# Kernel tuning notes

Hardware: AMD Instinct MI355X
Metric: run time of the kernel (lower is better)

The kernel has to match this reference:

```python
import jax, jax.numpy as jnp
import numpy as np
import math

D = 1024            # model dim
H = 4               # gru heads
HD = D // H         # 256 head dim
DI = int(HD * 1.5)  # 384 minGRU inner dim (expansion_factor=1.5)
FF_INNER = int(D * 4 * 2 / 3)  # 2730 SwiGLU inner
K = 4               # causal depthwise conv kernel
RES_SCALE = 1.0     # 1/sqrt(num_layers=1)


def setup_inputs() -> dict:
    key = jax.random.key(0)
    ks = jax.random.split(key, 12)
    s = lambda k, shape, sc: jax.random.normal(k, shape, jnp.float32) * sc
    return {
        "x": s(ks[0], (4, 4096, D), 1.0),
        "dw_w": s(ks[1], (D, 1, K), 0.3),
        "dw_b": jnp.zeros((D,), jnp.float32),
        "pw_w": s(ks[2], (D, D), 1.0 / math.sqrt(D)),
        "pw_b": jnp.zeros((D,), jnp.float32),
        "conv_gamma": jnp.zeros((D,), jnp.float32),
        "gru_gamma": jnp.zeros((D,), jnp.float32),
        "ff_gamma": jnp.zeros((D,), jnp.float32),
        "w_hg": s(ks[3], (H, HD, 2 * DI), 1.0 / math.sqrt(HD)),
        "w_out": s(ks[4], (H, DI, HD), 1.0 / math.sqrt(DI)),
        "w_gate": s(ks[5], (D, FF_INNER), 1.0 / math.sqrt(D)),
        "w_value": s(ks[6], (D, FF_INNER), 1.0 / math.sqrt(D)),
        "w_ff_out": s(ks[7], (FF_INNER, D), 1.0 / math.sqrt(FF_INNER)),
    }


def _rmsnorm(x, gamma):
    # F.normalize(x, dim=-1) * sqrt(dim) * (gamma + 1)
    n = jnp.sqrt(jnp.sum(x * x, axis=-1, keepdims=True))
    return x / jnp.maximum(n, 1e-12) * math.sqrt(x.shape[-1]) * (gamma + 1.0)


def _log_g(x):
    return jnp.where(x >= 0, jnp.log(jax.nn.relu(x) + 0.5), -jax.nn.softplus(-x))


def _causal_conv(x, dw_w, dw_b, pw_w, pw_b):
    # x: [B,L,D] -> causal depthwise conv (k=K) -> pointwise 1x1
    xt = jnp.transpose(x, (0, 2, 1))  # [B,D,L]
    xt = jnp.pad(xt, ((0, 0), (0, 0), (K - 1, 0)))
    y = jax.lax.conv_general_dilated(
        xt, dw_w, (1,), "VALID",
        dimension_numbers=("NCH", "OIH", "NCH"),
        feature_group_count=D) + dw_b[None, :, None]
    y = jnp.einsum("bdl,ed->bel", y, pw_w) + pw_b[None, :, None]
    return jnp.transpose(y, (0, 2, 1))


def reference(x, dw_w, dw_b, pw_w, pw_b, conv_gamma, gru_gamma, ff_gamma,
              w_hg, w_out, w_gate, w_value, w_ff_out):
    B, L, _ = x.shape
    # conv residual branch
    x = _causal_conv(_rmsnorm(x, conv_gamma), dw_w, dw_b, pw_w, pw_b) * RES_SCALE + x
    # multi-head minGRU (all heads vectorized; prev_hidden=None)
    normed = _rmsnorm(x, gru_gamma).reshape(B, L, H, HD)
    hg = jnp.einsum("blhd,hde->blhe", normed, w_hg)  # [B,L,H,2*DI]
    hidden, gate = hg[..., :DI], hg[..., DI:]
    log_coeffs = -jax.nn.softplus(gate)
    log_values = -jax.nn.softplus(-gate) + _log_g(hidden)
    # heinsen associative scan in log space along L
    a_star = jnp.cumsum(log_coeffs, axis=1)
    log_h = a_star + jax.lax.cumlogsumexp(log_values - a_star, axis=1)
    h = jnp.exp(log_h)  # [B,L,H,DI]
    next_hidden = h[:, -1:].reshape(B, 1, H * DI)
    gru_out = jnp.einsum("blhe,heo->blho", h, w_out).reshape(B, L, D)
    x = gru_out * RES_SCALE + x
    # SwiGLU FFN residual branch
    n = _rmsnorm(x, ff_gamma)
    ff = (jax.nn.silu(n @ w_gate) * (n @ w_value)) @ w_ff_out
    x = ff * RES_SCALE + x
    return x, next_hidden
```

## Files before the change

### kernel.cpp

```cpp
#include <hip/hip_runtime.h>
#include <stdint.h>


#define DM     1024
#define SEQL   4096
#define FFN    2730
#define FFP    2816
#define NH_OFF 16777216L
#define CHLEN  128

using bf16x8 = __attribute__((ext_vector_type(8))) short;
using f32x4  = __attribute__((ext_vector_type(4))) float;

__device__ __forceinline__ float bf2f(unsigned short h) {
  union { unsigned int u; float f; } v; v.u = ((unsigned int)h) << 16; return v.f;
}
__device__ __forceinline__ unsigned short f2bf(float f) {
  union { float f; unsigned int u; } v; v.f = f;
  unsigned int u = v.u;
  return (unsigned short)((u + 0x7fffu + ((u >> 16) & 1u)) >> 16);
}
__device__ __forceinline__ float ldin(const void* p, long i, int f32mode) {
  return f32mode ? ((const float*)p)[i] : bf2f(((const unsigned short*)p)[i]);
}
__device__ __forceinline__ void stout(void* p, long i, int f32mode, float v) {
  if (f32mode) ((float*)p)[i] = v; else ((unsigned short*)p)[i] = f2bf(v);
}
__device__ __forceinline__ void gload_lds16(const unsigned short* g, unsigned short* lds) {
  __builtin_amdgcn_global_load_lds(
      (const __attribute__((address_space(1))) unsigned int*)g,
      (__attribute__((address_space(3))) unsigned int*)lds,
      16, 0, 0);
}

__global__ void detect_k(const unsigned short* __restrict__ x, int* __restrict__ flag) {
  __shared__ int cnt;
  if (threadIdx.x == 0) cnt = 0;
  __syncthreads();
  int c = 0;
  for (int j = 0; j < 4; j++) {
    unsigned short v = x[2 * (threadIdx.x * 4 + j)];
    int ex = (v >> 7) & 0xFF;
    if (ex >= 0x84) c++;
  }
  atomicAdd(&cnt, c);
  __syncthreads();
  if (threadIdx.x == 0) *flag = (cnt >= 32) ? 1 : 0;
}

template <int EPI>
__launch_bounds__(256)
__global__ void gemm_bf16(const unsigned short* __restrict__ A, int lda, int aOffZ,
                          const unsigned short* __restrict__ Bm, int bOffZ, int K,
                          void* __restrict__ Cout, int ldc, int cOffZ, long outOff,
                          const unsigned short* __restrict__ bias,
                          const void* __restrict__ res, int ldres, long resOff,
                          const int* __restrict__ flagp) {
  __shared__ __align__(16) unsigned short As[128][64];
  __shared__ __align__(16) unsigned short Bs[128][64];

  const int tid  = threadIdx.x;
  const int w    = tid >> 6;
  const int lane = tid & 63;
  const int z    = blockIdx.z;
  const long tm  = (long)blockIdx.y * 128;
  const long tn  = (long)blockIdx.x * 128;

  const unsigned short* Ag = A + (long)z * aOffZ;
  const unsigned short* Bg = Bm + (long)z * bOffZ;

  f32x4 acc[4][4];
#pragma unroll
  for (int i = 0; i < 4; i++)
#pragma unroll
    for (int j = 0; j < 4; j++) acc[i][j] = (f32x4){0.f, 0.f, 0.f, 0.f};

  const int wrow = w * 32;
  const int srow = lane >> 3;
  const int scol = (((lane & 7) ^ srow) * 8);
  const int wm   = (w >> 1) * 64;
  const int wn   = (w & 1) * 64;
  const int quad = lane >> 4;
  const int lo   = lane & 15;
  const int sw   = lo & 7;

  for (int k0 = 0; k0 < K; k0 += 64) {
    __syncthreads();
#pragma unroll
    for (int i = 0; i < 4; i++) {
      const int r = wrow + i * 8;
      gload_lds16(Ag + (tm + r + srow) * (long)lda + k0 + scol, &As[r][0]);
      gload_lds16(Bg + (tn + r + srow) * (long)K + k0 + scol, &Bs[r][0]);
    }
    __syncthreads();
#pragma unroll
    for (int kk = 0; kk < 64; kk += 32) {
      const int kc = kk >> 3;
      bf16x8 af[4], bfr[4];
#pragma unroll
      for (int mt = 0; mt < 4; mt++)
        af[mt] = *(const bf16x8*)&As[wm + mt * 16 + lo][((quad + kc) ^ sw) * 8];
#pragma unroll
      for (int nt = 0; nt < 4; nt++)
        bfr[nt] = *(const bf16x8*)&Bs[wn + nt * 16 + lo][((quad + kc) ^ sw) * 8];
#pragma unroll
      for (int mt = 0; mt < 4; mt++)
#pragma unroll
        for (int nt = 0; nt < 4; nt++)
          acc[mt][nt] = __builtin_amdgcn_mfma_f32_16x16x32_bf16(af[mt], bfr[nt], acc[mt][nt], 0, 0, 0);
    }
  }

  const int f32m = (EPI == 1 || EPI == 3) ? *flagp : 0;
#pragma unroll
  for (int mt = 0; mt < 4; mt++) {
#pragma unroll
    for (int nt = 0; nt < 4; nt++) {
#pragma unroll
      for (int r = 0; r < 4; r++) {
        const long grow = tm + wm + mt * 16 + quad * 4 + r;
        const long gcol = tn + wn + nt * 16 + lo;
        float v         = acc[mt][nt][r];
        if (EPI == 0) {
          ((unsigned short*)Cout + (long)z * cOffZ)[grow * (long)ldc + gcol] = f2bf(v);
        } else if (EPI == 1) {
          v += bf2f(bias[gcol]) + ldin(res, resOff + grow * (long)ldres + gcol, f32m);
          ((unsigned short*)Cout)[grow * (long)ldc + gcol] = f2bf(v);
        } else if (EPI == 2) {
          v += bf2f(((const unsigned short*)res + (long)z * cOffZ)[grow * (long)ldres + gcol]);
          ((unsigned short*)Cout + (long)z * cOffZ)[grow * (long)ldc + gcol] = f2bf(v);
        } else {
          v += bf2f(((const unsigned short*)res)[grow * (long)ldres + gcol]);
          stout(Cout, outOff + grow * (long)ldc + gcol, f32m, v);
        }
      }
    }
  }
}

__launch_bounds__(256)
__global__ void gemm_ff(const unsigned short* __restrict__ A,
                        const unsigned short* __restrict__ Bgm,
                        const unsigned short* __restrict__ Bvm,
                        unsigned short* __restrict__ Cout) {
  __shared__ __align__(16) unsigned short As[128][64];
  __shared__ __align__(16) unsigned short Bgs[128][64];
  __shared__ __align__(16) unsigned short Bvs[128][64];

  const int tid  = threadIdx.x;
  const int w    = tid >> 6;
  const int lane = tid & 63;
  const long tm  = (long)blockIdx.y * 128;
  const long tn  = (long)blockIdx.x * 128;

  f32x4 accG[4][4], accV[4][4];
#pragma unroll
  for (int i = 0; i < 4; i++)
#pragma unroll
    for (int j = 0; j < 4; j++) {
      accG[i][j] = (f32x4){0.f, 0.f, 0.f, 0.f};
      accV[i][j] = (f32x4){0.f, 0.f, 0.f, 0.f};
    }

  const int wrow = w * 32;
  const int srow = lane >> 3;
  const int scol = (((lane & 7) ^ srow) * 8);
  const int wm   = (w >> 1) * 64;
  const int wn   = (w & 1) * 64;
  const int quad = lane >> 4;
  const int lo   = lane & 15;
  const int sw   = lo & 7;

  for (int k0 = 0; k0 < DM; k0 += 64) {
    __syncthreads();
#pragma unroll
    for (int i = 0; i < 4; i++) {
      const int r = wrow + i * 8;
      gload_lds16(A + (tm + r + srow) * (long)DM + k0 + scol, &As[r][0]);
      gload_lds16(Bgm + (tn + r + srow) * (long)DM + k0 + scol, &Bgs[r][0]);
      gload_lds16(Bvm + (tn + r + srow) * (long)DM + k0 + scol, &Bvs[r][0]);
    }
    __syncthreads();
#pragma unroll
    for (int kk = 0; kk < 64; kk += 32) {
      const int kc = kk >> 3;
      bf16x8 af[4], bfr[4];
#pragma unroll
      for (int mt = 0; mt < 4; mt++)
        af[mt] = *(const bf16x8*)&As[wm + mt * 16 + lo][((quad + kc) ^ sw) * 8];
#pragma unroll
      for (int nt = 0; nt < 4; nt++)
        bfr[nt] = *(const bf16x8*)&Bgs[wn + nt * 16 + lo][((quad + kc) ^ sw) * 8];
#pragma unroll
      for (int mt = 0; mt < 4; mt++)
#pragma unroll
        for (int nt = 0; nt < 4; nt++)
          accG[mt][nt] = __builtin_amdgcn_mfma_f32_16x16x32_bf16(af[mt], bfr[nt], accG[mt][nt], 0, 0, 0);
#pragma unroll
      for (int nt = 0; nt < 4; nt++)
        bfr[nt] = *(const bf16x8*)&Bvs[wn + nt * 16 + lo][((quad + kc) ^ sw) * 8];
#pragma unroll
      for (int mt = 0; mt < 4; mt++)
#pragma unroll
        for (int nt = 0; nt < 4; nt++)
          accV[mt][nt] = __builtin_amdgcn_mfma_f32_16x16x32_bf16(af[mt], bfr[nt], accV[mt][nt], 0, 0, 0);
    }
  }

#pragma unroll
  for (int mt = 0; mt < 4; mt++) {
#pragma unroll
    for (int nt = 0; nt < 4; nt++) {
#pragma unroll
      for (int r = 0; r < 4; r++) {
        const long grow = tm + wm + mt * 16 + quad * 4 + r;
        const long gcol = tn + wn + nt * 16 + lo;
        const float g   = accG[mt][nt][r];
        const float s   = g / (1.f + __expf(-g));
        Cout[grow * (long)FFP + gcol] = f2bf(s * accV[mt][nt][r]);
      }
    }
  }
}

template <int EPI>
__launch_bounds__(512, 2)
__global__ void gemm256(const unsigned short* __restrict__ A,
                        const unsigned short* __restrict__ Bm,
                        int K,
                        void* __restrict__ Cout,
                        const unsigned short* __restrict__ res,
                        long outOff,
                        const int* __restrict__ flagp) {
  __shared__ __align__(16) unsigned short As[2][256][64];
  __shared__ __align__(16) unsigned short Bs[2][256][64];

  const int tid  = threadIdx.x;
  const int w    = tid >> 6;
  const int lane = tid & 63;
  const int wr   = w >> 2;
  const int wc   = w & 3;
  const int quad = lane >> 4;
  const int lo   = lane & 15;
  const int sw   = lo & 7;

  const int gx  = gridDim.x;
  int bid       = blockIdx.y * gx + blockIdx.x;
  const int nwg = gx * gridDim.y;
  {
    const int q = nwg >> 3, r8 = nwg & 7;
    const int xc8 = bid & 7, j = bid >> 3;
    bid = (xc8 < r8 ? xc8 * (q + 1) : r8 * (q + 1) + (xc8 - r8) * q) + j;
  }
  const long tn = (long)(bid % gx) * 256;
  const long tm = (long)(bid / gx) * 256;

  const int NT = K >> 6;

  const int srow = lane >> 3;
  const int sch  = (lane & 7) ^ srow;
  const unsigned short* Ab = A + (tm + (long)w * 8 + srow) * (long)K + sch * 8;
  const unsigned short* Bb = Bm + (tn + (long)w * 8 + srow) * (long)K + sch * 8;

#define STAGE_A(BUF, TT, G) \
  gload_lds16(Ab + (long)((G) * 64) * K + (long)(TT) * 64, &As[BUF][(G) * 64 + w * 8][0])
#define STAGE_B(BUF, TT, G) \
  gload_lds16(Bb + (long)((G) * 64) * K + (long)(TT) * 64, &Bs[BUF][(G) * 64 + w * 8][0])

  STAGE_A(0, 0, 0); STAGE_A(0, 0, 2);
  STAGE_B(0, 0, 0); STAGE_B(0, 0, 1);
  STAGE_A(0, 0, 1); STAGE_A(0, 0, 3);
  STAGE_B(0, 0, 2); STAGE_B(0, 0, 3);
  STAGE_A(1, 1, 0); STAGE_A(1, 1, 2);
  STAGE_B(1, 1, 0); STAGE_B(1, 1, 1);
  STAGE_A(1, 1, 1); STAGE_A(1, 1, 3);

  f32x4 acc[8][4];
#pragma unroll
  for (int i = 0; i < 8; i++)
#pragma unroll
    for (int j = 0; j < 4; j++) acc[i][j] = (f32x4){0.f, 0.f, 0.f, 0.f};

  asm volatile("s_waitcnt vmcnt(6)" ::: "memory");
  __builtin_amdgcn_s_barrier();

  bf16x8 a[4][2], b[4][2];

#define LDA256(CBUF, base_row)                                                    \
  _Pragma("unroll") for (int m = 0; m < 4; m++) {                                 \
    _Pragma("unroll") for (int c = 0; c < 2; c++) {                               \
      a[m][c] = *(const bf16x8*)&As[CBUF][(base_row) + m * 16 + lo]               \
                                       [((quad + 4 * c) ^ sw) * 8];               \
    }                                                                             \
  }
#define LDB256(CBUF, nb)                                                          \
  _Pragma("unroll") for (int n = 0; n < 2; n++) {                                 \
    _Pragma("unroll") for (int c = 0; c < 2; c++) {                               \
      b[(nb) + n][c] = *(const bf16x8*)&Bs[CBUF][wc * 64 + ((nb) + n) * 16 + lo]  \
                                              [((quad + 4 * c) ^ sw) * 8];        \
    }                                                                             \
  }
#define MFMA16(MB, NB)                                                            \
  __builtin_amdgcn_s_setprio(1);                                                  \
  _Pragma("unroll") for (int m = 0; m < 4; m++) {                                 \
    _Pragma("unroll") for (int n = 0; n < 2; n++) {                               \
      _Pragma("unroll") for (int c = 0; c < 2; c++) {                             \
        acc[(MB) + m][(NB) + n] = __builtin_amdgcn_mfma_f32_16x16x32_bf16(        \
            a[m][c], b[(NB) + n][c], acc[(MB) + m][(NB) + n], 0, 0, 0);           \
      }                                                                           \
    }                                                                             \
  }                                                                               \
  __builtin_amdgcn_s_setprio(0);

#define SUBTILE(CBUF, TT, ST1, ST2, LAST)                                         \
  {                                                                               \
                                                                         \
    LDA256(CBUF, wr * 128);                                                       \
    LDB256(CBUF, 0);                                                              \
    if (ST1) { STAGE_B(CBUF ^ 1, (TT) + 1, 2); STAGE_B(CBUF ^ 1, (TT) + 1, 3); }  \
    MFMA16(0, 0);                                                                 \
    __builtin_amdgcn_s_barrier();                                                 \
                                                                         \
    LDB256(CBUF, 2);                                                              \
    if (ST2) { STAGE_A(CBUF, (TT) + 2, 0); STAGE_A(CBUF, (TT) + 2, 2); }          \
    MFMA16(0, 2);                                                                 \
    __builtin_amdgcn_s_barrier();                                                 \
                                                                         \
    LDA256(CBUF, wr * 128 + 64);                                                  \
    if (ST2) { STAGE_B(CBUF, (TT) + 2, 0); STAGE_B(CBUF, (TT) + 2, 1); }          \
    MFMA16(4, 2);                                                                 \
    __builtin_amdgcn_s_barrier();                                                 \
                                                                         \
    if (ST2) { STAGE_A(CBUF, (TT) + 2, 1); STAGE_A(CBUF, (TT) + 2, 3); }          \
    MFMA16(4, 0);                                                                 \
    if (LAST) asm volatile("s_waitcnt vmcnt(0)" ::: "memory");                    \
    else      asm volatile("s_waitcnt vmcnt(6)" ::: "memory");                    \
    __builtin_amdgcn_s_barrier();                                                 \
  }

  for (int t = 0; t + 3 < NT; t += 2) {
    SUBTILE(0, t, 1, 1, 0)
    SUBTILE(1, t + 1, 1, 1, 0)
  }
  SUBTILE(0, NT - 2, 1, 0, 1)
  SUBTILE(1, NT - 1, 0, 0, 1)

  if (EPI == 0) {
    const long colb = (tn >> 1);
    const long rowb = tm + wr * 128;
#pragma unroll
    for (int m = 0; m < 8; m++) {
#pragma unroll
      for (int np = 0; np < 2; np++) {
        const long col = colb + (wc * 2 + np) * 16 + lo;
#pragma unroll
        for (int r = 0; r < 4; r++) {
          const long row = rowb + m * 16 + quad * 4 + r;
          const float g  = acc[m][2 * np][r];
          const float v  = acc[m][2 * np + 1][r];
          const float s  = g / (1.f + __expf(-g));
          ((unsigned short*)Cout)[row * (long)FFP + col] = f2bf(s * v);
        }
      }
    }
  } else {
    const int f32m = *flagp;
    const long rowb = tm + wr * 128;
    const long colb = tn + wc * 64;
#pragma unroll
    for (int m = 0; m < 8; m++) {
#pragma unroll
      for (int n = 0; n < 4; n++) {
#pragma unroll
        for (int r = 0; r < 4; r++) {
          const long row = rowb + m * 16 + quad * 4 + r;
          const long col = colb + n * 16 + lo;
          float v = acc[m][n][r] + bf2f(res[row * (long)DM + col]);
          stout(Cout, outOff + row * (long)DM + col, f32m, v);
        }
      }
    }
  }
#undef STAGE_A
#undef STAGE_B
#undef LDA256
#undef LDB256
#undef MFMA16
#undef SUBTILE
}

__global__ void rmsnorm_x(const void* __restrict__ in, long elemOff,
                          const unsigned short* __restrict__ gamma,
                          unsigned short* __restrict__ out,
                          const int* __restrict__ flagp) {
  const int t    = blockIdx.x;
  const int lane = threadIdx.x;
  const int f32m = *flagp;
  float v[16];
  const long base = elemOff + (long)t * DM;
  if (f32m) {
    const float4* rp = (const float4*)((const float*)in + base);
#pragma unroll
    for (int j = 0; j < 4; j++) {
      float4 u     = rp[j * 64 + lane];
      v[j * 4 + 0] = u.x; v[j * 4 + 1] = u.y; v[j * 4 + 2] = u.z; v[j * 4 + 3] = u.w;
    }
  } else {
    const ushort4* rp = (const ushort4*)((const unsigned short*)in + base);
#pragma unroll
    for (int j = 0; j < 4; j++) {
      ushort4 u    = rp[j * 64 + lane];
      v[j * 4 + 0] = bf2f(u.x); v[j * 4 + 1] = bf2f(u.y);
      v[j * 4 + 2] = bf2f(u.z); v[j * 4 + 3] = bf2f(u.w);
    }
  }
  float s = 0.f;
#pragma unroll
  for (int i = 0; i < 16; i++) s = fmaf(v[i], v[i], s);
#pragma unroll
  for (int off = 32; off > 0; off >>= 1) s += __shfl_xor(s, off, 64);
  const float scale = 32.f / fmaxf(sqrtf(s), 1e-12f);
  ushort4* op       = (ushort4*)(out + (long)t * DM);
  const ushort4* gp = (const ushort4*)gamma;
#pragma unroll
  for (int j = 0; j < 4; j++) {
    ushort4 g = gp[j * 64 + lane];
    ushort4 o;
    o.x = f2bf(v[j * 4 + 0] * scale * (bf2f(g.x) + 1.f));
    o.y = f2bf(v[j * 4 + 1] * scale * (bf2f(g.y) + 1.f));
    o.z = f2bf(v[j * 4 + 2] * scale * (bf2f(g.z) + 1.f));
    o.w = f2bf(v[j * 4 + 3] * scale * (bf2f(g.w) + 1.f));
    op[j * 64 + lane] = o;
  }
}

__global__ void rmsnorm_k(const unsigned short* __restrict__ in,
                          const unsigned short* __restrict__ gamma,
                          unsigned short* __restrict__ out) {
  const int t    = blockIdx.x;
  const int lane = threadIdx.x;
  float v[16];
  const ushort4* rp = (const ushort4*)(in + (long)t * DM);
#pragma unroll
  for (int j = 0; j < 4; j++) {
    ushort4 u    = rp[j * 64 + lane];
    v[j * 4 + 0] = bf2f(u.x); v[j * 4 + 1] = bf2f(u.y);
    v[j * 4 + 2] = bf2f(u.z); v[j * 4 + 3] = bf2f(u.w);
  }
  float s = 0.f;
#pragma unroll
  for (int i = 0; i < 16; i++) s = fmaf(v[i], v[i], s);
#pragma unroll
  for (int off = 32; off > 0; off >>= 1) s += __shfl_xor(s, off, 64);
  const float scale = 32.f / fmaxf(sqrtf(s), 1e-12f);
  ushort4* op       = (ushort4*)(out + (long)t * DM);
  const ushort4* gp = (const ushort4*)gamma;
#pragma unroll
  for (int j = 0; j < 4; j++) {
    ushort4 g = gp[j * 64 + lane];
    ushort4 o;
    o.x = f2bf(v[j * 4 + 0] * scale * (bf2f(g.x) + 1.f));
    o.y = f2bf(v[j * 4 + 1] * scale * (bf2f(g.y) + 1.f));
    o.z = f2bf(v[j * 4 + 2] * scale * (bf2f(g.z) + 1.f));
    o.w = f2bf(v[j * 4 + 3] * scale * (bf2f(g.w) + 1.f));
    op[j * 64 + lane] = o;
  }
}

__global__ void dwconv_k(const unsigned short* __restrict__ xn,
                         const unsigned short* __restrict__ dww,
                         const unsigned short* __restrict__ dwb,
                         unsigned short* __restrict__ y, int l0) {
  const int t = blockIdx.x;
  const int d = blockIdx.y * 256 + threadIdx.x;
  const int l = l0 + (t & (SEQL - 1));
  ushort4 w4  = ((const ushort4*)dww)[d];
  float wk[4] = {bf2f(w4.x), bf2f(w4.y), bf2f(w4.z), bf2f(w4.w)};
  float acc   = bf2f(dwb[d]);
#pragma unroll
  for (int k = 0; k < 4; k++) {
    const int ll = l + k - 3;
    if (ll >= 0) acc = fmaf(bf2f(xn[(long)(t + k - 3) * DM + d]), wk[k], acc);
  }
  y[(long)t * DM + d] = f2bf(acc);
}

__device__ __forceinline__ void cv_compute(float gt, float& c, float& sg) {
  gt = fminf(fmaxf(gt, -40.f), 40.f);
  const float e  = __expf(-fabsf(gt));
  const float r  = 1.f / (1.f + e);
  const float rs = e * r;
  c  = (gt >= 0.f) ? rs : r;
  sg = (gt >= 0.f) ? r : rs;
}
__device__ __forceinline__ float gfun(float hid) {
  hid = fminf(fmaxf(hid, -40.f), 40.f);
  if (hid >= 0.f) return hid + 0.5f;
  const float e = __expf(hid);
  return e / (1.f + e);
}

__global__ void scan_p1(const unsigned short* __restrict__ hg, float* __restrict__ cC,
                        float* __restrict__ cV, int chTot, int SL) {
  const int e = threadIdx.x, bh = blockIdx.y, cid = blockIdx.x;
  const int bL = bh >> 2, hh = bh & 3;
  long base = ((long)(bL * SL + cid * CHLEN)) * 3072 + hh * 768 + e;
  float C = 1.f, V = 0.f;
  for (int i = 0; i < CHLEN; i++) {
    const float hid = bf2f(hg[base]), gt = bf2f(hg[base + 384]);
    float c, sg; cv_compute(gt, c, sg);
    C *= c;
    V = fmaf(c, V, sg * gfun(hid));
    base += 3072;
  }
  const int idx = cid * chTot + bh * 384 + e;
  cC[idx] = C; cV[idx] = V;
}

__global__ void scan_p2(const float* __restrict__ cC, const float* __restrict__ cV,
                        float* __restrict__ hin, int chTot, int CHNp,
                        const float* __restrict__ hcarry, int useCarry) {
  const int ch = blockIdx.x * 384 + threadIdx.x;
  float h = useCarry ? hcarry[ch] : 0.f;
  for (int cid = 0; cid < CHNp; cid++) {
    const int idx = cid * chTot + ch;
    hin[idx] = h;
    h = fmaf(cC[idx], h, cV[idx]);
  }
}

__global__ void scan_p3(const unsigned short* __restrict__ hg, const float* __restrict__ hin,
                        unsigned short* __restrict__ hout, void* __restrict__ nh, long nhOff,
                        float* __restrict__ hcarry, int chTot, int SL, int CHNp,
                        int writeNh, const int* __restrict__ flagp) {
  const int e = threadIdx.x, bh = blockIdx.y, cid = blockIdx.x;
  const int bL = bh >> 2, hh = bh & 3;
  const long tok = (long)bL * SL + (long)cid * CHLEN;
  long base  = tok * 3072 + hh * 768 + e;
  long obase = tok * 1536 + hh * 384 + e;
  float h = hin[cid * chTot + bh * 384 + e];
  for (int i = 0; i < CHLEN; i++) {
    const float hid = bf2f(hg[base]), gt = bf2f(hg[base + 384]);
    float c, sg; cv_compute(gt, c, sg);
    h = fmaf(c, h, sg * gfun(hid));
    hout[obase] = f2bf(h);
    base += 3072; obase += 1536;
  }
  if (cid == CHNp - 1) {
    hcarry[bh * 384 + e] = h;
    if (writeNh) stout(nh, nhOff + bL * 1536 + hh * 384 + e, *flagp, h);
  }
}

__global__ void cvt_k(const void* __restrict__ in, unsigned short* __restrict__ out,
                      int n, const int* __restrict__ flagp) {
  const int i = blockIdx.x * 256 + threadIdx.x;
  if (i < n) out[i] = f2bf(ldin(in, i, *flagp));
}
__global__ void tr_whg(const void* __restrict__ in, unsigned short* __restrict__ out,
                       const int* __restrict__ flagp) {
  const int idx = blockIdx.x * 256 + threadIdx.x;
  const int k = idx & 255, n = (idx >> 8) % 768, h = idx / (768 * 256);
  out[idx] = f2bf(ldin(in, (long)(h * 256 + k) * 768 + n, *flagp));
}
__global__ void tr_wout(const void* __restrict__ in, unsigned short* __restrict__ out,
                        const int* __restrict__ flagp) {
  const int idx = blockIdx.x * 256 + threadIdx.x;
  const int k = idx % 384, n = (idx / 384) & 255, h = idx / (384 * 256);
  out[idx] = f2bf(ldin(in, (long)(h * 384 + k) * 256 + n, *flagp));
}
__global__ void tr_wg(const void* __restrict__ in, unsigned short* __restrict__ out,
                      const int* __restrict__ flagp) {
  const int idx = blockIdx.x * 256 + threadIdx.x;
  const int k = idx & 1023, n = idx >> 10;
  out[idx] = (n < FFN) ? f2bf(ldin(in, (long)k * FFN + n, *flagp)) : (unsigned short)0;
}
__global__ void tr_wgv(const void* __restrict__ wg, const void* __restrict__ wv,
                       unsigned short* __restrict__ out, const int* __restrict__ flagp) {
  const int idx = blockIdx.x * 256 + threadIdx.x;
  const int k = idx & 1023, R = idx >> 10;
  const int tile = R >> 8, rb = R & 255;
  const int pair = rb >> 5, sel = (rb >> 4) & 1, r16 = rb & 15;
  const int col  = tile * 128 + pair * 16 + r16;
  const void* src = sel ? wv : wg;
  out[idx] = (col < FFN) ? f2bf(ldin(src, (long)k * FFN + col, *flagp)) : (unsigned short)0;
}
__global__ void tr_wfo(const void* __restrict__ in, unsigned short* __restrict__ out,
                       const int* __restrict__ flagp) {
  const int idx = blockIdx.x * 256 + threadIdx.x;
  const int kk = idx % FFP, n = idx / FFP;
  out[idx] = (kk < FFN) ? f2bf(ldin(in, (long)kk * DM + n, *flagp)) : (unsigned short)0;
}

extern "C" void kernel_launch(void* const* d_in, const int* in_sizes, int n_in,
                              void* d_out, int out_size, void* d_ws, size_t ws_size,
                              hipStream_t stream) {
  const void* x      = d_in[0];
  const void* dw_w   = d_in[1];
  const void* dw_b   = d_in[2];
  const void* pw_w   = d_in[3];
  const void* pw_b   = d_in[4];
  const void* conv_g = d_in[5];
  const void* gru_g  = d_in[6];
  const void* ff_g   = d_in[7];
  const void* w_hg   = d_in[8];
  const void* w_out  = d_in[9];
  const void* w_gate = d_in[10];
  const void* w_val  = d_in[11];
  const void* w_ffo  = d_in[12];

  const long FIXED = 21795072L;
  int MT = 128;
  if      (ws_size >= (size_t)(FIXED + 16384L * 13888)) MT = 16384;
  else if (ws_size >= (size_t)(FIXED + 8192L * 13888))  MT = 8192;
  else if (ws_size >= (size_t)(FIXED + 4096L * 13888))  MT = 4096;
  else if (ws_size >= (size_t)(FIXED + 2048L * 13888))  MT = 2048;
  else if (ws_size >= (size_t)(FIXED + 1024L * 13888))  MT = 1024;
  else if (ws_size >= (size_t)(FIXED + 512L * 13888))   MT = 512;
  else if (ws_size >= (size_t)(FIXED + 256L * 13888))   MT = 256;

  const int SL    = (MT >= SEQL) ? SEQL : MT;
  const int nSeq  = MT / SL;
  const int CHNp  = SL / CHLEN;
  const int chTot = nSeq * 1536;
  const int big   = (MT >= 256);

  char* p = (char*)d_ws;
  unsigned short* whgT  = (unsigned short*)p; p += 1572864;
  unsigned short* woutT = (unsigned short*)p; p += 786432;
  unsigned short* wgT   = (unsigned short*)p; p += 5767168;
  unsigned short* wvT   = (unsigned short*)p; p += 5767168;
  unsigned short* wfoT  = (unsigned short*)p; p += 5767168;
  unsigned short* pwT   = (unsigned short*)p; p += 2097152;
  unsigned short* dwwB  = (unsigned short*)p; p += 8192;
  unsigned short* dwbB  = (unsigned short*)p; p += 2048;
  unsigned short* pwbB  = (unsigned short*)p; p += 2048;
  unsigned short* cgB   = (unsigned short*)p; p += 2048;
  unsigned short* ggB   = (unsigned short*)p; p += 2048;
  unsigned short* fgB   = (unsigned short*)p; p += 2048;
  int*            flag  = (int*)p;            p += 256;
  float*          hcarry= (float*)p;          p += 12288;
  float*          cC    = (float*)p;          p += (long)MT * 192;
  float*          cV    = (float*)p;          p += (long)MT * 192;
  float*          hin   = (float*)p;          p += (long)MT * 192;
  unsigned short* xnb   = (unsigned short*)p; p += 6144 + (long)MT * 2048;
  unsigned short* xc    = (unsigned short*)p; p += (long)MT * 2048;
  unsigned short* hbuf  = (unsigned short*)p; p += (long)MT * 3072;
  unsigned short* ybuf  = (unsigned short*)p;
  unsigned short* hg    = (unsigned short*)p;
  unsigned short* ffin  = (unsigned short*)p;
  unsigned short* xn    = xnb + 3 * DM;
  unsigned short* wgvT  = wgT;

  detect_k<<<1, 256, 0, stream>>>((const unsigned short*)x, flag);
  tr_whg<<<3072, 256, 0, stream>>>(w_hg, whgT, flag);
  tr_wout<<<1536, 256, 0, stream>>>(w_out, woutT, flag);
  if (big) {
    tr_wgv<<<22528, 256, 0, stream>>>(w_gate, w_val, wgvT, flag);
  } else {
    tr_wg<<<11264, 256, 0, stream>>>(w_gate, wgT, flag);
    tr_wg<<<11264, 256, 0, stream>>>(w_val, wvT, flag);
  }
  tr_wfo<<<11264, 256, 0, stream>>>(w_ffo, wfoT, flag);
  cvt_k<<<4096, 256, 0, stream>>>(pw_w, pwT, 1048576, flag);
  cvt_k<<<16, 256, 0, stream>>>(dw_w, dwwB, 4096, flag);
  cvt_k<<<4, 256, 0, stream>>>(dw_b, dwbB, 1024, flag);
  cvt_k<<<4, 256, 0, stream>>>(pw_b, pwbB, 1024, flag);
  cvt_k<<<4, 256, 0, stream>>>(conv_g, cgB, 1024, flag);
  cvt_k<<<4, 256, 0, stream>>>(gru_g, ggB, 1024, flag);
  cvt_k<<<4, 256, 0, stream>>>(ff_g, fgB, 1024, flag);

  for (long t0 = 0; t0 < 16384; t0 += MT) {
    const int l0     = (int)(t0 & (SEQL - 1));
    const int P      = (l0 > 0) ? 3 : 0;
    const int seqEnd = (l0 + SL == SEQL);
    const long nhOff = NH_OFF + (t0 / SEQL) * 1536;

    rmsnorm_x<<<MT + P, 64, 0, stream>>>(x, (t0 - P) * DM, cgB, xn - (long)P * DM, flag);
    dwconv_k<<<dim3(MT, 4), 256, 0, stream>>>(xn, dwwB, dwbB, ybuf, l0);
    gemm_bf16<1><<<dim3(8, MT / 128, 1), 256, 0, stream>>>(ybuf, DM, 0, pwT, 0, DM,
        xc, DM, 0, 0L, pwbB, x, DM, t0 * DM, flag);

    rmsnorm_k<<<MT, 64, 0, stream>>>(xc, ggB, xn);
    gemm_bf16<0><<<dim3(6, MT / 128, 4), 256, 0, stream>>>(xn, DM, 256, whgT, 196608, 256,
        hg, 3072, 768, 0L, nullptr, nullptr, 0, 0L, nullptr);
    scan_p1<<<dim3(CHNp, nSeq * 4), 384, 0, stream>>>(hg, cC, cV, chTot, SL);
    scan_p2<<<nSeq * 4, 384, 0, stream>>>(cC, cV, hin, chTot, CHNp, hcarry, l0 > 0);
    scan_p3<<<dim3(CHNp, nSeq * 4), 384, 0, stream>>>(hg, hin, hbuf, d_out, nhOff,
        hcarry, chTot, SL, CHNp, seqEnd, flag);
    gemm_bf16<2><<<dim3(2, MT / 128, 4), 256, 0, stream>>>(hbuf, 1536, 384, woutT, 98304, 384,
        xc, DM, 256, 0L, nullptr, xc, DM, 0L, nullptr);

    rmsnorm_k<<<MT, 64, 0, stream>>>(xc, fgB, xn);
    if (big) {
      gemm256<0><<<dim3(22, MT / 256), 512, 0, stream>>>(xn, wgvT, DM,
          ffin, nullptr, 0L, nullptr);
      gemm256<1><<<dim3(4, MT / 256), 512, 0, stream>>>(ffin, wfoT, FFP,
          d_out, xc, t0 * DM, flag);
    } else {
      gemm_ff<<<dim3(22, MT / 128), 256, 0, stream>>>(xn, wgT, wvT, ffin);
      gemm_bf16<3><<<dim3(8, MT / 128, 1), 256, 0, stream>>>(ffin, FFP, 0, wfoT, 0, FFP,
          d_out, DM, 0, t0 * DM, nullptr, xc, DM, 0L, flag);
    }
  }
}
```

Before: 975.2 us.

## Restructure GEMM main loop to prefetch LDS fragments across subtiles

Reworks the 256x256 GEMM inner loop to keep separate A-low, A-high and two B fragment register sets. Each quarter's LDS reads are issued while the previous quarter's MFMAs run, and the next buffer's first fragments are prefetched at the end of each subtile. Global-to-LDS staging is reordered so whole A then whole B tiles land per phase, with adjusted vmcnt waits. This aims to hide LDS read latency behind MFMA work, at the cost of more VGPRs and more delicate wait/barrier ordering.

```diff
diff --git a/kernel.cpp b/kernel.cpp
--- a/kernel.cpp
+++ b/kernel.cpp
@@ -268,12 +268,11 @@
   gload_lds16(Bb + (long)((G) * 64) * K + (long)(TT) * 64, &Bs[BUF][(G) * 64 + w * 8][0])
 
   STAGE_A(0, 0, 0); STAGE_A(0, 0, 2);
-  STAGE_B(0, 0, 0); STAGE_B(0, 0, 1);
   STAGE_A(0, 0, 1); STAGE_A(0, 0, 3);
-  STAGE_B(0, 0, 2); STAGE_B(0, 0, 3);
+  STAGE_B(0, 0, 0); STAGE_B(0, 0, 1); STAGE_B(0, 0, 2); STAGE_B(0, 0, 3);
   STAGE_A(1, 1, 0); STAGE_A(1, 1, 2);
-  STAGE_B(1, 1, 0); STAGE_B(1, 1, 1);
   STAGE_A(1, 1, 1); STAGE_A(1, 1, 3);
+  STAGE_B(1, 1, 0); STAGE_B(1, 1, 1); STAGE_B(1, 1, 2); STAGE_B(1, 1, 3);
 
   f32x4 acc[8][4];
 #pragma unroll
@@ -281,69 +280,91 @@
 #pragma unroll
     for (int j = 0; j < 4; j++) acc[i][j] = (f32x4){0.f, 0.f, 0.f, 0.f};
 
-  asm volatile("s_waitcnt vmcnt(6)" ::: "memory");
+  asm volatile("s_waitcnt vmcnt(8)" ::: "memory");
   __builtin_amdgcn_s_barrier();
 
-  bf16x8 a[4][2], b[4][2];
-
-#define LDA256(CBUF, base_row)                                                    \
+  bf16x8 aL[4][2], aH[4][2], b01[2][2], b23[2][2];
+
+#define LDAL(CBUF)                                                                \
   _Pragma("unroll") for (int m = 0; m < 4; m++) {                                 \
     _Pragma("unroll") for (int c = 0; c < 2; c++) {                               \
-      a[m][c] = *(const bf16x8*)&As[CBUF][(base_row) + m * 16 + lo]               \
-                                       [((quad + 4 * c) ^ sw) * 8];               \
+      aL[m][c] = *(const bf16x8*)&As[CBUF][wr * 128 + m * 16 + lo]                \
+                                        [((quad + 4 * c) ^ sw) * 8];              \
     }                                                                             \
   }
-#define LDB256(CBUF, nb)                                                          \
+#define LDAH(CBUF)                                                                \
+  _Pragma("unroll") for (int m = 0; m < 4; m++) {                                 \
+    _Pragma("unroll") for (int c = 0; c < 2; c++) {                               \
+      aH[m][c] = *(const bf16x8*)&As[CBUF][wr * 128 + 64 + m * 16 + lo]           \
+                                        [((quad + 4 * c) ^ sw) * 8];              \
+    }                                                                             \
+  }
+#define LDB01(CBUF)                                                               \
   _Pragma("unroll") for (int n = 0; n < 2; n++) {                                 \
     _Pragma("unroll") for (int c = 0; c < 2; c++) {                               \
-      b[(nb) + n][c] = *(const bf16x8*)&Bs[CBUF][wc * 64 + ((nb) + n) * 16 + lo]  \
-                                              [((quad + 4 * c) ^ sw) * 8];        \
+      b01[n][c] = *(const bf16x8*)&Bs[CBUF][wc * 64 + n * 16 + lo]                \
+                                         [((quad + 4 * c) ^ sw) * 8];             \
     }                                                                             \
   }
-#define MFMA16(MB, NB)                                                            \
+#define LDB23(CBUF)                                                               \
+  _Pragma("unroll") for (int n = 0; n < 2; n++) {                                 \
+    _Pragma("unroll") for (int c = 0; c < 2; c++) {                               \
+      b23[n][c] = *(const bf16x8*)&Bs[CBUF][wc * 64 + 32 + n * 16 + lo]           \
+                                         [((quad + 4 * c) ^ sw) * 8];             \
+    }                                                                             \
+  }
+#define MFMA_Q(MB, AF, NB, BF)                                                    \
   __builtin_amdgcn_s_setprio(1);                                                  \
   _Pragma("unroll") for (int m = 0; m < 4; m++) {                                 \
     _Pragma("unroll") for (int n = 0; n < 2; n++) {                               \
       _Pragma("unroll") for (int c = 0; c < 2; c++) {                             \
         acc[(MB) + m][(NB) + n] = __builtin_amdgcn_mfma_f32_16x16x32_bf16(        \
-            a[m][c], b[(NB) + n][c], acc[(MB) + m][(NB) + n], 0, 0, 0);           \
+            AF[m][c], BF[n][c], acc[(MB) + m][(NB) + n], 0, 0, 0);                \
       }                                                                           \
     }                                                                             \
   }                                                                               \
   __builtin_amdgcn_s_setprio(0);
 
-#define SUBTILE(CBUF, TT, ST1, ST2, LAST)                                         \
+#define LGKM0 asm volatile("s_waitcnt lgkmcnt(0)" ::: "memory")
+
+#define SUBTILE(CBUF, TT, STG, PRF, VM)                                           \
   {                                                                               \
-                                                                         \
-    LDA256(CBUF, wr * 128);                                                       \
-    LDB256(CBUF, 0);                                                              \
-    if (ST1) { STAGE_B(CBUF ^ 1, (TT) + 1, 2); STAGE_B(CBUF ^ 1, (TT) + 1, 3); }  \
-    MFMA16(0, 0);                                                                 \
+                                                            \
+    LGKM0;                                                                        \
+    if (STG) { STAGE_A(CBUF, (TT) + 2, 0); STAGE_A(CBUF, (TT) + 2, 2); }          \
+    MFMA_Q(0, aL, 0, b01);                                                        \
+    LDAH(CBUF);                                                                   \
     __builtin_amdgcn_s_barrier();                                                 \
-                                                                         \
-    LDB256(CBUF, 2);                                                              \
-    if (ST2) { STAGE_A(CBUF, (TT) + 2, 0); STAGE_A(CBUF, (TT) + 2, 2); }          \
-    MFMA16(0, 2);                                                                 \
+                                                            \
+    LGKM0;                                                                        \
+    if (STG) { STAGE_A(CBUF, (TT) + 2, 1); STAGE_A(CBUF, (TT) + 2, 3); }          \
+    MFMA_Q(4, aH, 0, b01);                                                        \
+    LDB23(CBUF);                                                                  \
+    if ((VM) == 4) asm volatile("s_waitcnt vmcnt(4)" ::: "memory");               \
+    else if ((VM) == 0) asm volatile("s_waitcnt vmcnt(0)" ::: "memory");          \
     __builtin_amdgcn_s_barrier();                                                 \
-                                                                         \
-    LDA256(CBUF, wr * 128 + 64);                                                  \
-    if (ST2) { STAGE_B(CBUF, (TT) + 2, 0); STAGE_B(CBUF, (TT) + 2, 1); }          \
-    MFMA16(4, 2);                                                                 \
+                                                            \
+    LGKM0;                                                                        \
+    if (STG) { STAGE_B(CBUF, (TT) + 2, 0); STAGE_B(CBUF, (TT) + 2, 1);            \
+               STAGE_B(CBUF, (TT) + 2, 2); STAGE_B(CBUF, (TT) + 2, 3); }          \
+    MFMA_Q(0, aL, 2, b23);                                                        \
+    if (PRF) LDB01(CBUF ^ 1);                                                     \
     __builtin_amdgcn_s_barrier();                                                 \
-                                                                         \
-    if (ST2) { STAGE_A(CBUF, (TT) + 2, 1); STAGE_A(CBUF, (TT) + 2, 3); }          \
-    MFMA16(4, 0);                                                                 \
-    if (LAST) asm volatile("s_waitcnt vmcnt(0)" ::: "memory");                    \
-    else      asm volatile("s_waitcnt vmcnt(6)" ::: "memory");                    \
+                        \
+    MFMA_Q(4, aH, 2, b23);                                                        \
+    if (PRF) LDAL(CBUF ^ 1);                                                      \
     __builtin_amdgcn_s_barrier();                                                 \
   }
 
+  LDB01(0);
+  LDAL(0);
+
   for (int t = 0; t + 3 < NT; t += 2) {
-    SUBTILE(0, t, 1, 1, 0)
-    SUBTILE(1, t + 1, 1, 1, 0)
-  }
-  SUBTILE(0, NT - 2, 1, 0, 1)
-  SUBTILE(1, NT - 1, 0, 0, 1)
+    SUBTILE(0, t, 1, 1, 4)
+    SUBTILE(1, t + 1, 1, 1, 4)
+  }
+  SUBTILE(0, NT - 2, 0, 1, 0)
+  SUBTILE(1, NT - 1, 0, 0, -1)
 
   if (EPI == 0) {
     const long colb = (tn >> 1);
@@ -383,9 +404,12 @@
   }
 #undef STAGE_A
 #undef STAGE_B
-#undef LDA256
-#undef LDB256
-#undef MFMA16
+#undef LDAL
+#undef LDAH
+#undef LDB01
+#undef LDB23
+#undef MFMA_Q
+#undef LGKM0
 #undef SUBTILE
 }
 
```

New measurement: 1.063 ms. +9.0%, slower.

## Halve K-tile in gemm256 to 32 and raise occupancy to four blocks

Applied to the files above, without the earlier changes.

The 256x256 GEMM now stages K slices of 32 instead of 64, which halves LDS use per block. It uses a new 4-way XOR swizzle and a reworked two-phase pipeline with fewer barriers per tile. Launch bounds are raised to 4 blocks per CU so more workgroups can be resident. The trade-off is twice as many loop iterations and barriers relative to compute, plus register pressure from the 32 accumulators per thread under the tighter bound.

```diff
diff --git a/kernel.cpp b/kernel.cpp
--- a/kernel.cpp
+++ b/kernel.cpp
@@ -224,7 +224,7 @@
 }
 
 template <int EPI>
-__launch_bounds__(512, 2)
+__launch_bounds__(512, 4)
 __global__ void gemm256(const unsigned short* __restrict__ A,
                         const unsigned short* __restrict__ Bm,
                         int K,
@@ -232,8 +232,8 @@
                         const unsigned short* __restrict__ res,
                         long outOff,
                         const int* __restrict__ flagp) {
-  __shared__ __align__(16) unsigned short As[2][256][64];
-  __shared__ __align__(16) unsigned short Bs[2][256][64];
+  __shared__ __align__(16) unsigned short As[2][256][32];
+  __shared__ __align__(16) unsigned short Bs[2][256][32];
 
   const int tid  = threadIdx.x;
   const int w    = tid >> 6;
@@ -242,7 +242,7 @@
   const int wc   = w & 3;
   const int quad = lane >> 4;
   const int lo   = lane & 15;
-  const int sw   = lo & 7;
+  const int rkey = ((lo & 3) ^ (lo >> 2)) & 3;
 
   const int gx  = gridDim.x;
   int bid       = blockIdx.y * gx + blockIdx.x;
@@ -255,25 +255,22 @@
   const long tn = (long)(bid % gx) * 256;
   const long tm = (long)(bid / gx) * 256;
 
-  const int NT = K >> 6;
-
-  const int srow = lane >> 3;
-  const int sch  = (lane & 7) ^ srow;
-  const unsigned short* Ab = A + (tm + (long)w * 8 + srow) * (long)K + sch * 8;
-  const unsigned short* Bb = Bm + (tn + (long)w * 8 + srow) * (long)K + sch * 8;
+  const int NT = K >> 5;
+
+  const int srow = lane >> 2;
+  const int spos = lane & 3;
+  const int skey = ((srow & 3) ^ (srow >> 2)) & 3;
+  const unsigned short* Ab = A + (tm + (long)w * 16 + srow) * (long)K + (spos ^ skey) * 8;
+  const unsigned short* Bb = Bm + (tn + (long)w * 16 + srow) * (long)K + (spos ^ skey) * 8;
 
 #define STAGE_A(BUF, TT, G) \
-  gload_lds16(Ab + (long)((G) * 64) * K + (long)(TT) * 64, &As[BUF][(G) * 64 + w * 8][0])
+  gload_lds16(Ab + (long)((G) * 128) * K + (long)(TT) * 32, &As[BUF][(G) * 128 + w * 16][0])
 #define STAGE_B(BUF, TT, G) \
-  gload_lds16(Bb + (long)((G) * 64) * K + (long)(TT) * 64, &Bs[BUF][(G) * 64 + w * 8][0])
-
-  STAGE_A(0, 0, 0); STAGE_A(0, 0, 2);
+  gload_lds16(Bb + (long)((G) * 128) * K + (long)(TT) * 32, &Bs[BUF][(G) * 128 + w * 16][0])
+
   STAGE_B(0, 0, 0); STAGE_B(0, 0, 1);
-  STAGE_A(0, 0, 1); STAGE_A(0, 0, 3);
-  STAGE_B(0, 0, 2); STAGE_B(0, 0, 3);
-  STAGE_A(1, 1, 0); STAGE_A(1, 1, 2);
+  STAGE_A(0, 0, 0); STAGE_A(0, 0, 1);
   STAGE_B(1, 1, 0); STAGE_B(1, 1, 1);
-  STAGE_A(1, 1, 1); STAGE_A(1, 1, 3);
 
   f32x4 acc[8][4];
 #pragma unroll
@@ -281,69 +278,54 @@
 #pragma unroll
     for (int j = 0; j < 4; j++) acc[i][j] = (f32x4){0.f, 0.f, 0.f, 0.f};
 
-  asm volatile("s_waitcnt vmcnt(6)" ::: "memory");
+  asm volatile("s_waitcnt vmcnt(2)" ::: "memory");
   __builtin_amdgcn_s_barrier();
 
-  bf16x8 a[4][2], b[4][2];
-
-#define LDA256(CBUF, base_row)                                                    \
+  bf16x8 aF[4], bF[4];
+
+#define LDA4(CBUF, MB)                                                            \
   _Pragma("unroll") for (int m = 0; m < 4; m++) {                                 \
-    _Pragma("unroll") for (int c = 0; c < 2; c++) {                               \
-      a[m][c] = *(const bf16x8*)&As[CBUF][(base_row) + m * 16 + lo]               \
-                                       [((quad + 4 * c) ^ sw) * 8];               \
-    }                                                                             \
-  }
-#define LDB256(CBUF, nb)                                                          \
-  _Pragma("unroll") for (int n = 0; n < 2; n++) {                                 \
-    _Pragma("unroll") for (int c = 0; c < 2; c++) {                               \
-      b[(nb) + n][c] = *(const bf16x8*)&Bs[CBUF][wc * 64 + ((nb) + n) * 16 + lo]  \
-                                              [((quad + 4 * c) ^ sw) * 8];        \
-    }                                                                             \
-  }
-#define MFMA16(MB, NB)                                                            \
+    aF[m] = *(const bf16x8*)&As[CBUF][wr * 128 + ((MB) + m) * 16 + lo]            \
+                                    [(quad ^ rkey) * 8];                          \
+  }
+#define LDB4(CBUF)                                                                \
+  _Pragma("unroll") for (int n = 0; n < 4; n++) {                                 \
+    bF[n] = *(const bf16x8*)&Bs[CBUF][wc * 64 + n * 16 + lo]                      \
+                                    [(quad ^ rkey) * 8];                          \
+  }
+#define MFMA16(MB)                                                                \
   __builtin_amdgcn_s_setprio(1);                                                  \
   _Pragma("unroll") for (int m = 0; m < 4; m++) {                                 \
-    _Pragma("unroll") for (int n = 0; n < 2; n++) {                               \
-      _Pragma("unroll") for (int c = 0; c < 2; c++) {                             \
-        acc[(MB) + m][(NB) + n] = __builtin_amdgcn_mfma_f32_16x16x32_bf16(        \
-            a[m][c], b[(NB) + n][c], acc[(MB) + m][(NB) + n], 0, 0, 0);           \
-      }                                                                           \
+    _Pragma("unroll") for (int n = 0; n < 4; n++) {                               \
+      acc[(MB) + m][n] = __builtin_amdgcn_mfma_f32_16x16x32_bf16(                 \
+          aF[m], bF[n], acc[(MB) + m][n], 0, 0, 0);                               \
     }                                                                             \
   }                                                                               \
   __builtin_amdgcn_s_setprio(0);
 
-#define SUBTILE(CBUF, TT, ST1, ST2, LAST)                                         \
+#define SUBTILE(CBUF, TT, SA, SB, VM)                                             \
   {                                                                               \
-                                                                         \
-    LDA256(CBUF, wr * 128);                                                       \
-    LDB256(CBUF, 0);                                                              \
-    if (ST1) { STAGE_B(CBUF ^ 1, (TT) + 1, 2); STAGE_B(CBUF ^ 1, (TT) + 1, 3); }  \
-    MFMA16(0, 0);                                                                 \
+             \
+    LDA4(CBUF, 0);                                                                \
+    LDB4(CBUF);                                                                   \
+    if (SA) { STAGE_A(CBUF ^ 1, (TT) + 1, 0); STAGE_A(CBUF ^ 1, (TT) + 1, 1); }   \
+    MFMA16(0);                                                                    \
     __builtin_amdgcn_s_barrier();                                                 \
-                                                                         \
-    LDB256(CBUF, 2);                                                              \
-    if (ST2) { STAGE_A(CBUF, (TT) + 2, 0); STAGE_A(CBUF, (TT) + 2, 2); }          \
-    MFMA16(0, 2);                                                                 \
+           \
+    LDA4(CBUF, 4);                                                                \
+    if (SB) { STAGE_B(CBUF, (TT) + 2, 0); STAGE_B(CBUF, (TT) + 2, 1); }           \
+    MFMA16(4);                                                                    \
+    if ((VM) == 2) asm volatile("s_waitcnt vmcnt(2)" ::: "memory");               \
+    else if ((VM) == 0) asm volatile("s_waitcnt vmcnt(0)" ::: "memory");          \
     __builtin_amdgcn_s_barrier();                                                 \
-                                                                         \
-    LDA256(CBUF, wr * 128 + 64);                                                  \
-    if (ST2) { STAGE_B(CBUF, (TT) + 2, 0); STAGE_B(CBUF, (TT) + 2, 1); }          \
-    MFMA16(4, 2);                                                                 \
-    __builtin_amdgcn_s_barrier();                                                 \
-                                                                         \
-    if (ST2) { STAGE_A(CBUF, (TT) + 2, 1); STAGE_A(CBUF, (TT) + 2, 3); }          \
-    MFMA16(4, 0);                                                                 \
-    if (LAST) asm volatile("s_waitcnt vmcnt(0)" ::: "memory");                    \
-    else      asm volatile("s_waitcnt vmcnt(6)" ::: "memory");                    \
-    __builtin_amdgcn_s_barrier();                                                 \
   }
 
   for (int t = 0; t + 3 < NT; t += 2) {
-    SUBTILE(0, t, 1, 1, 0)
-    SUBTILE(1, t + 1, 1, 1, 0)
-  }
-  SUBTILE(0, NT - 2, 1, 0, 1)
-  SUBTILE(1, NT - 1, 0, 0, 1)
+    SUBTILE(0, t, 1, 1, 2)
+    SUBTILE(1, t + 1, 1, 1, 2)
+  }
+  SUBTILE(0, NT - 2, 1, 0, 0)
+  SUBTILE(1, NT - 1, 0, 0, -1)
 
   if (EPI == 0) {
     const long colb = (tn >> 1);
@@ -383,8 +365,8 @@
   }
 #undef STAGE_A
 #undef STAGE_B
-#undef LDA256
-#undef LDB256
+#undef LDA4
+#undef LDB4
 #undef MFMA16
 #undef SUBTILE
 }
```

After: 3.727 ms. +282.2%, slower.
